# Kernel tuning notes

Measured on AMD Instinct MI355X. Metric: run time of the kernel, lower is better.

Reference implementation:

```python
import jax, jax.numpy as jnp
import numpy as np

B, C, T, F = 16, 64, 400, 64
H = C          # GRU hidden == numUnits == channel
G = 8          # PE groups


def _gru(xs, Wih, Whh, bih, bhh):
    """PyTorch-style GRU, batch_first. xs: [N, T, I]; Wih: [3H, I]; Whh: [3H, H]."""
    gx = jnp.einsum('nti,gi->ntg', xs, Wih) + bih          # [N, T, 3H] input gates precomputed
    Hh = Whh.shape[1]

    def step(h, gxt):
        gh = h @ Whh.T + bhh                               # [N, 3H]
        xr, xz, xn = jnp.split(gxt, 3, axis=-1)
        hr, hz, hn = jnp.split(gh, 3, axis=-1)
        r = jax.nn.sigmoid(xr + hr)
        z = jax.nn.sigmoid(xz + hz)
        n = jnp.tanh(xn + r * hn)
        hn_new = (1.0 - z) * n + z * h
        return hn_new, hn_new

    h0 = jnp.zeros((xs.shape[0], Hh), xs.dtype)
    _, ys = jax.lax.scan(step, h0, jnp.swapaxes(gx, 0, 1))
    return jnp.swapaxes(ys, 0, 1)                          # [N, T, H]


def _ln2(x, g, b, eps=1e-8):
    """LayerNorm over last two dims [width, numUnits]."""
    mu = x.mean(axis=(-2, -1), keepdims=True)
    var = x.var(axis=(-2, -1), keepdims=True)
    return (x - mu) / jnp.sqrt(var + eps) * g + b


def setup_inputs() -> dict:
    key = jax.random.key(0)
    ks = jax.random.split(key, 24)
    s = 0.1

    def rn(k, shape):
        return jax.random.normal(k, shape, dtype=jnp.float32) * s

    return {
        'x': jax.random.normal(ks[0], (B, C, T, F), dtype=jnp.float32),
        # intra bidirectional GRU (input = C = H)
        'intra_Wih_f': rn(ks[1], (3 * H, H)), 'intra_Whh_f': rn(ks[2], (3 * H, H)),
        'intra_bih_f': rn(ks[3], (3 * H,)),   'intra_bhh_f': rn(ks[4], (3 * H,)),
        'intra_Wih_b': rn(ks[5], (3 * H, H)), 'intra_Whh_b': rn(ks[6], (3 * H, H)),
        'intra_bih_b': rn(ks[7], (3 * H,)),   'intra_bhh_b': rn(ks[8], (3 * H,)),
        'intra_fc_W': rn(ks[9], (H, 2 * H)),  'intra_fc_b': rn(ks[10], (H,)),
        'intra_ln_g': jnp.ones((F, H), jnp.float32), 'intra_ln_b': jnp.zeros((F, H), jnp.float32),
        # PE: 8 grouped GRUs + FCs (stacked along group axis)
        'pe_Wih': rn(ks[11], (G, 3 * H, H)), 'pe_Whh': rn(ks[12], (G, 3 * H, H)),
        'pe_bih': rn(ks[13], (G, 3 * H)),    'pe_bhh': rn(ks[14], (G, 3 * H)),
        'pe_fc_W': rn(ks[15], (G, H, H)),    'pe_fc_b': rn(ks[16], (G, H)),
        'pe_ln_g': jnp.ones((F, H), jnp.float32), 'pe_ln_b': jnp.zeros((F, H), jnp.float32),
    }


def _forward(x, intra_Wih_f, intra_Whh_f, intra_bih_f, intra_bhh_f,
             intra_Wih_b, intra_Whh_b, intra_bih_b, intra_bhh_b,
             intra_fc_W, intra_fc_b, intra_ln_g, intra_ln_b,
             pe_Wih, pe_Whh, pe_bih, pe_bhh, pe_fc_W, pe_fc_b, pe_ln_g, pe_ln_b):
    b, c, t, f = x.shape
    xp = jnp.transpose(x, (0, 2, 3, 1))                    # [b, t, f, c]

    # ---- intra path: bidirectional GRU along frequency f ----
    seq = xp.reshape(b * t, f, c)
    fwd = _gru(seq, intra_Wih_f, intra_Whh_f, intra_bih_f, intra_bhh_f)
    bwd = jnp.flip(_gru(jnp.flip(seq, 1), intra_Wih_b, intra_Whh_b, intra_bih_b, intra_bhh_b), 1)
    intra = jnp.concatenate([fwd, bwd], axis=-1) @ intra_fc_W.T + intra_fc_b
    intra = _ln2(intra.reshape(b, t, f, c), intra_ln_g, intra_ln_b)
    intra_out = xp + intra                                  # residual

    # ---- PE: 8 grouped GRUs along time t ----
    y = jnp.transpose(intra_out, (0, 2, 1, 3))             # [b, f, t, c]
    fg = f // G
    yg = y.reshape(b, G, fg, t, c)                         # chunk freq into G groups
    yg = jnp.transpose(yg, (1, 0, 2, 3, 4)).reshape(G, b * fg, t, c)
    rnn = jax.vmap(_gru)(yg, pe_Wih, pe_Whh, pe_bih, pe_bhh)    # [G, b*fg, t, H]
    fc = jnp.einsum('gnth,goh->gnto', rnn, pe_fc_W) + pe_fc_b[:, None, None, :]
    fc = fc.reshape(G, b, fg, t, H).transpose(1, 0, 2, 3, 4).reshape(b, f, t, H)
    inter = _ln2(jnp.transpose(fc, (0, 2, 1, 3)), pe_ln_g, pe_ln_b)   # [b, t, f, c]

    out = intra + inter                                     # note: residual with intra (pre-add), per source
    return jnp.transpose(out, (0, 3, 1, 2))                 # [b, c, t, f]


def reference(x, intra_Wih_f, intra_Whh_f, intra_bih_f, intra_bhh_f,
              intra_Wih_b, intra_Whh_b, intra_bih_b, intra_bhh_b,
              intra_fc_W, intra_fc_b, intra_ln_g, intra_ln_b,
              pe_Wih, pe_Whh, pe_bih, pe_bhh, pe_fc_W, pe_fc_b, pe_ln_g, pe_ln_b):
    return _forward(x, intra_Wih_f, intra_Whh_f, intra_bih_f, intra_bhh_f,
                    intra_Wih_b, intra_Whh_b, intra_bih_b, intra_bhh_b,
                    intra_fc_W, intra_fc_b, intra_ln_g, intra_ln_b,
                    pe_Wih, pe_Whh, pe_bih, pe_bhh, pe_fc_W, pe_fc_b, pe_ln_g, pe_ln_b)
```

## Files before the change

### kernel.cpp

```cpp
#include <hip/hip_runtime.h>
#include <hip/hip_bf16.h>

typedef unsigned short u16;
typedef __attribute__((ext_vector_type(8))) short short8;
typedef __attribute__((ext_vector_type(4))) float f32x4;

#define MFMA16(A,B,C) __builtin_amdgcn_mfma_f32_16x16x32_bf16((A),(B),(C),0,0,0)

#define LDS_FENCE_ACQ()  asm volatile("s_waitcnt lgkmcnt(0)" ::: "memory")
#define LDS_FENCE_REL()  asm volatile("" ::: "memory")

__device__ __forceinline__ float bf2f(u16 u){ return __uint_as_float(((unsigned)u)<<16); }
__device__ __forceinline__ u16 f2bf(float f){
  unsigned x = __float_as_uint(f);
  return (u16)((x + 0x7FFFu + ((x>>16)&1u)) >> 16);
}
__device__ __forceinline__ float sigm(float x){ return __fdividef(1.f, 1.f + __expf(-x)); }
__device__ __forceinline__ float tanh_(float x){ return __fdividef(2.f, 1.f + __expf(-2.f*x)) - 1.f; }
__device__ __forceinline__ short8 ldg8(const u16* p){ return *(const short8*)p; }

struct CvtArgs {
  const void* src[21];
  u16* dst[21];
  int n[21];
};

__global__ __launch_bounds__(256,1) void k_cvt(CvtArgs a)
{
  const u16* d = (const u16*)a.src[0];
  int imp = 0, pl = 0;
#pragma unroll
  for (int i = 0; i < 128; i += 2){
    u16 u = d[i]; int e = (u >> 7) & 0xFF;
    if (u){ if (e >= 104 && e <= 134) pl++; else imp++; }
  }
  bool isf32 = imp > pl;

  int which, i0, stride;
  if (blockIdx.x < 20){ which = blockIdx.x + 1; i0 = threadIdx.x; stride = 256; }
  else { which = 0; i0 = (blockIdx.x - 20)*256 + threadIdx.x; stride = (gridDim.x - 20)*256; }
  int n = a.n[which];
  u16* dst = a.dst[which];
  if (isf32){
    const float* s = (const float*)a.src[which];
    for (int i = i0; i < n; i += stride) dst[i] = f2bf(s[i]);
  } else {
    const u16* s = (const u16*)a.src[which];
    for (int i = i0; i < n; i += stride) dst[i] = s[i];
  }
}

__global__ __launch_bounds__(256,1) void k_transpose(const u16* __restrict__ x, u16* __restrict__ xp)
{
  int nb = blockIdx.x; int b = nb/400, t = nb - b*400;
  int tid = threadIdx.x;
  __shared__ u16 tl[64*66];
  int f0 = (tid & 31) * 2;
#pragma unroll
  for (int p = 0; p < 8; p++){
    int c = p*8 + (tid>>5);
    unsigned u = *(const unsigned*)(x + (((size_t)b*64 + c)*400 + t)*64 + f0);
    *(unsigned*)(tl + c*66 + f0) = u;
  }
  __syncthreads();
  int c0 = (tid & 31) * 2;
  u16* dst = xp + (size_t)nb*4096;
#pragma unroll
  for (int p = 0; p < 8; p++){
    int f = p*8 + (tid>>5);
    unsigned u = (unsigned)tl[c0*66 + f] | ((unsigned)tl[(c0+1)*66 + f] << 16);
    *(unsigned*)(dst + f*64 + c0) = u;
  }
}

__global__ __launch_bounds__(64,1) void k_intra(
    const u16* __restrict__ xp,
    const u16* __restrict__ Wih_f, const u16* __restrict__ Whh_f,
    const u16* __restrict__ bih_f, const u16* __restrict__ bhh_f,
    const u16* __restrict__ Wih_b, const u16* __restrict__ Whh_b,
    const u16* __restrict__ bih_b, const u16* __restrict__ bhh_b,
    u16* __restrict__ yfo, u16* __restrict__ ybo)
{
  int blk = blockIdx.x;
  int dir = blk >= 400;
  int tile = dir ? blk - 400 : blk;
  int n0 = tile * 16;
  const u16* Wih = dir ? Wih_b : Wih_f;
  const u16* Whh = dir ? Whh_b : Whh_f;
  const u16* bih = dir ? bih_b : bih_f;
  const u16* bhh = dir ? bhh_b : bhh_f;
  u16* yo = dir ? ybo : yfo;

  int lane = threadIdx.x;
  int m = lane & 15, q = lane >> 4;

  short8 wrx[4][2], wzx[4][2], wnx[4][2], wrh[4][2], wzh[4][2], wnh[4][2];
#pragma unroll
  for (int nt = 0; nt < 4; nt++){
#pragma unroll
    for (int kc = 0; kc < 2; kc++){
      int co = kc*32 + q*8;
      wrx[nt][kc] = ldg8(Wih + (      nt*16 + m)*64 + co);
      wzx[nt][kc] = ldg8(Wih + ( 64 + nt*16 + m)*64 + co);
      wnx[nt][kc] = ldg8(Wih + (128 + nt*16 + m)*64 + co);
      wrh[nt][kc] = ldg8(Whh + (      nt*16 + m)*64 + co);
      wzh[nt][kc] = ldg8(Whh + ( 64 + nt*16 + m)*64 + co);
      wnh[nt][kc] = ldg8(Whh + (128 + nt*16 + m)*64 + co);
    }
  }
  float br[4], bz[4], bnx_[4], bnh_[4];
#pragma unroll
  for (int nt = 0; nt < 4; nt++){
    int u = nt*16 + m;
    br[nt]   = bf2f(bih[u])     + bf2f(bhh[u]);
    bz[nt]   = bf2f(bih[64+u])  + bf2f(bhh[64+u]);
    bnx_[nt] = bf2f(bih[128+u]);
    bnh_[nt] = bf2f(bhh[128+u]);
  }

  __shared__ u16 hl[16*72];
  float h[4][4];
#pragma unroll
  for (int nt=0;nt<4;nt++){
#pragma unroll
    for (int p=0;p<4;p++) h[nt][p] = 0.f;
  }
  short8 hf0 = {0,0,0,0,0,0,0,0}, hf1 = {0,0,0,0,0,0,0,0};
  int f = dir ? 63 : 0, df = dir ? -1 : 1;
  short8 xf0 = ldg8(xp + ((size_t)(n0+m)*64 + f)*64 + q*8);
  short8 xf1 = ldg8(xp + ((size_t)(n0+m)*64 + f)*64 + 32 + q*8);

  for (int s = 0; s < 64; s++){
    f32x4 ar[4], az[4], anx[4], anh[4];
#pragma unroll
    for (int nt=0;nt<4;nt++){
      ar[nt]  = (f32x4){br[nt],br[nt],br[nt],br[nt]};
      az[nt]  = (f32x4){bz[nt],bz[nt],bz[nt],bz[nt]};
      anx[nt] = (f32x4){bnx_[nt],bnx_[nt],bnx_[nt],bnx_[nt]};
      anh[nt] = (f32x4){bnh_[nt],bnh_[nt],bnh_[nt],bnh_[nt]};
    }
#pragma unroll
    for (int nt=0;nt<4;nt++){
      ar[nt]  = MFMA16(hf0, wrh[nt][0], ar[nt]);
      ar[nt]  = MFMA16(hf1, wrh[nt][1], ar[nt]);
      ar[nt]  = MFMA16(xf0, wrx[nt][0], ar[nt]);
      ar[nt]  = MFMA16(xf1, wrx[nt][1], ar[nt]);
      az[nt]  = MFMA16(hf0, wzh[nt][0], az[nt]);
      az[nt]  = MFMA16(hf1, wzh[nt][1], az[nt]);
      az[nt]  = MFMA16(xf0, wzx[nt][0], az[nt]);
      az[nt]  = MFMA16(xf1, wzx[nt][1], az[nt]);
      anx[nt] = MFMA16(xf0, wnx[nt][0], anx[nt]);
      anx[nt] = MFMA16(xf1, wnx[nt][1], anx[nt]);
      anh[nt] = MFMA16(hf0, wnh[nt][0], anh[nt]);
      anh[nt] = MFMA16(hf1, wnh[nt][1], anh[nt]);
    }
    int fn = f + df;
    if (s < 63){
      xf0 = ldg8(xp + ((size_t)(n0+m)*64 + fn)*64 + q*8);
      xf1 = ldg8(xp + ((size_t)(n0+m)*64 + fn)*64 + 32 + q*8);
    }
#pragma unroll
    for (int nt=0;nt<4;nt++){
#pragma unroll
      for (int p=0;p<4;p++){
        float r  = sigm(ar[nt][p]);
        float z  = sigm(az[nt][p]);
        float n  = tanh_(anx[nt][p] + r*anh[nt][p]);
        float hn = n + z*(h[nt][p] - n);
        h[nt][p] = hn;
        hl[(q*4+p)*72 + nt*16 + m] = f2bf(hn);
      }
    }
    LDS_FENCE_ACQ();
    int sl = lane >> 2, ch = lane & 3;
    short8 y0 = *(const short8*)(hl + sl*72 + ch*16);
    short8 y1 = *(const short8*)(hl + sl*72 + ch*16 + 8);
    *(short8*)(yo + ((size_t)(n0+sl)*64 + f)*64 + ch*16)     = y0;
    *(short8*)(yo + ((size_t)(n0+sl)*64 + f)*64 + ch*16 + 8) = y1;
    hf0 = *(const short8*)(hl + m*72 + q*8);
    hf1 = *(const short8*)(hl + m*72 + 32 + q*8);
    LDS_FENCE_REL();
    f = fn;
  }
}

__global__ __launch_bounds__(256,1) void k_ifc(
  const u16* __restrict__ yf, const u16* __restrict__ yb,
  const u16* __restrict__ fcw, const u16* __restrict__ fcb,
  const u16* __restrict__ lng, const u16* __restrict__ lnb,
  const u16* __restrict__ xp, u16* __restrict__ lnI, u16* __restrict__ iout)
{
  int nb = blockIdx.x; int b = nb/400, t = nb - b*400;
  int tid = threadIdx.x; int wv = tid>>6; int lane = tid&63;
  int m = lane&15, q = lane>>4;
  int rb = nb*64 + wv*16;
  short8 a0 = ldg8(yf + (size_t)(rb+m)*64 + q*8);
  short8 a1 = ldg8(yf + (size_t)(rb+m)*64 + 32 + q*8);
  short8 a2 = ldg8(yb + (size_t)(rb+m)*64 + q*8);
  short8 a3 = ldg8(yb + (size_t)(rb+m)*64 + 32 + q*8);
  f32x4 acc[4];
#pragma unroll
  for (int nt=0;nt<4;nt++){
    float bias = bf2f(fcb[nt*16+m]);
    acc[nt] = (f32x4){bias,bias,bias,bias};
    acc[nt] = MFMA16(a0, ldg8(fcw + (nt*16+m)*128 +      q*8), acc[nt]);
    acc[nt] = MFMA16(a1, ldg8(fcw + (nt*16+m)*128 + 32 + q*8), acc[nt]);
    acc[nt] = MFMA16(a2, ldg8(fcw + (nt*16+m)*128 + 64 + q*8), acc[nt]);
    acc[nt] = MFMA16(a3, ldg8(fcw + (nt*16+m)*128 + 96 + q*8), acc[nt]);
  }
  float s=0.f, s2=0.f;
#pragma unroll
  for (int nt=0;nt<4;nt++){
#pragma unroll
    for (int p=0;p<4;p++){ float v=acc[nt][p]; s+=v; s2+=v*v; }
  }
  for (int o=32;o>0;o>>=1){ s += __shfl_down(s,o); s2 += __shfl_down(s2,o); }
  __shared__ float red[8];
  if (lane==0){ red[wv]=s; red[4+wv]=s2; }
  __syncthreads();
  float S  = red[0]+red[1]+red[2]+red[3];
  float S2 = red[4]+red[5]+red[6]+red[7];
  float mu = S*(1.f/4096.f);
  float rstd = rsqrtf(S2*(1.f/4096.f) - mu*mu + 1e-8f);
#pragma unroll
  for (int nt=0;nt<4;nt++){
#pragma unroll
    for (int p=0;p<4;p++){
      int row = wv*16 + q*4 + p;
      int col = nt*16 + m;
      float v = (acc[nt][p]-mu)*rstd;
      v = v*bf2f(lng[row*64+col]) + bf2f(lnb[row*64+col]);
      lnI[(size_t)nb*4096 + row*64 + col] = f2bf(v);
      float xv = bf2f(xp[(size_t)nb*4096 + row*64 + col]);
      iout[(((size_t)b*64 + row)*400 + t)*64 + col] = f2bf(v + xv);
    }
  }
}

__global__ __launch_bounds__(64,1) void k_gx(const u16* __restrict__ io,
   const u16* __restrict__ pw, const u16* __restrict__ pb, u16* __restrict__ gx)
{
  int r0 = blockIdx.x * 16;
  int seq = r0 / 400;
  int g = (seq & 63) >> 3;
  int lane = threadIdx.x; int m = lane&15, q = lane>>4;
  short8 a0 = ldg8(io + (size_t)(r0+m)*64 + q*8);
  short8 a1 = ldg8(io + (size_t)(r0+m)*64 + 32 + q*8);
  const u16* W = pw + g*12288;
#pragma unroll
  for (int nt=0; nt<12; nt++){
    float bias = bf2f(pb[g*192 + nt*16 + m]);
    f32x4 acc = (f32x4){bias,bias,bias,bias};
    acc = MFMA16(a0, ldg8(W + (nt*16+m)*64 + q*8), acc);
    acc = MFMA16(a1, ldg8(W + (nt*16+m)*64 + 32 + q*8), acc);
#pragma unroll
    for (int p=0;p<4;p++)
      gx[(size_t)(r0 + q*4 + p)*192 + nt*16 + m] = f2bf(acc[p]);
  }
}

__global__ __launch_bounds__(64,1) void k_pe(const u16* __restrict__ gx,
  const u16* __restrict__ whh, const u16* __restrict__ bhh, u16* __restrict__ ype)
{
  int seq = blockIdx.x;
  int g = (seq & 63) >> 3;
  int lane = threadIdx.x;
  int m = lane & 15, q = lane >> 4;

  const u16* W = whh + (size_t)g*12288;
  short8 wr[4][2], wz[4][2], wn[4][2];
#pragma unroll
  for (int nt = 0; nt < 4; nt++){
#pragma unroll
    for (int kc = 0; kc < 2; kc++){
      int co = kc*32 + q*8;
      wr[nt][kc] = ldg8(W + (      nt*16 + m)*64 + co);
      wz[nt][kc] = ldg8(W + ( 64 + nt*16 + m)*64 + co);
      wn[nt][kc] = ldg8(W + (128 + nt*16 + m)*64 + co);
    }
  }
  float br_[4], bz_[4], bn_[4];
#pragma unroll
  for (int nt = 0; nt < 4; nt++){
    br_[nt] = bf2f(bhh[g*192 +       nt*16 + m]);
    bz_[nt] = bf2f(bhh[g*192 + 64  + nt*16 + m]);
    bn_[nt] = bf2f(bhh[g*192 + 128 + nt*16 + m]);
  }

  const u16* gp = gx + (size_t)seq*400*192 + lane;
  u16* yp = ype + (size_t)seq*400*64 + lane;

  u16 cr0 = gp[0],   cz0 = gp[64],  cn0 = gp[128];
  u16 cr1 = gp[192], cz1 = gp[256], cn1 = gp[320];
  gp += 384;

  __shared__ __align__(16) u16 hbuf[128];

  float h = 0.f;
  short8 ah0 = {0,0,0,0,0,0,0,0}, ah1 = {0,0,0,0,0,0,0,0};
  short8 al0 = {0,0,0,0,0,0,0,0}, al1 = {0,0,0,0,0,0,0,0};

  f32x4 accr[4], accz[4], accn[4];
#pragma unroll
  for (int nt=0; nt<4; nt++){
    accr[nt] = (f32x4){br_[nt],br_[nt],br_[nt],br_[nt]};
    accz[nt] = (f32x4){bz_[nt],bz_[nt],bz_[nt],bz_[nt]};
    accn[nt] = (f32x4){bn_[nt],bn_[nt],bn_[nt],bn_[nt]};
  }

#define PE_STEP(CR, CZ, CN, PFOFF, COND)                                      \
  {                                                                           \
    float xr = bf2f(CR), xz = bf2f(CZ), xn = bf2f(CN);                        \
    if (COND){ CR = gp[PFOFF]; CZ = gp[(PFOFF)+64]; CN = gp[(PFOFF)+128]; }   \
    \
    \
    _Pragma("unroll")                                                         \
    for (int nt=0; nt<4; nt++){                                               \
      accr[nt][0] = br_[nt]; accz[nt][0] = bz_[nt]; accn[nt][0] = bn_[nt];    \
    }                                                                         \
    _Pragma("unroll")                                                         \
    for (int nt=0; nt<4; nt++){                                               \
      accr[nt] = MFMA16(ah0, wr[nt][0], accr[nt]);                            \
      accr[nt] = MFMA16(ah1, wr[nt][1], accr[nt]);                            \
      accr[nt] = MFMA16(al0, wr[nt][0], accr[nt]);                            \
      accr[nt] = MFMA16(al1, wr[nt][1], accr[nt]);                            \
      accz[nt] = MFMA16(ah0, wz[nt][0], accz[nt]);                            \
      accz[nt] = MFMA16(ah1, wz[nt][1], accz[nt]);                            \
      accz[nt] = MFMA16(al0, wz[nt][0], accz[nt]);                            \
      accz[nt] = MFMA16(al1, wz[nt][1], accz[nt]);                            \
      accn[nt] = MFMA16(ah0, wn[nt][0], accn[nt]);                            \
      accn[nt] = MFMA16(ah1, wn[nt][1], accn[nt]);                            \
      accn[nt] = MFMA16(al0, wn[nt][0], accn[nt]);                            \
      accn[nt] = MFMA16(al1, wn[nt][1], accn[nt]);                            \
    }                                                                         \
         \
    float ar = accr[0][0]; float az = accz[0][0]; float an = accn[0][0];      \
    ar = (q==1) ? accr[1][0] : ar; az = (q==1) ? accz[1][0] : az;             \
    an = (q==1) ? accn[1][0] : an;                                            \
    ar = (q==2) ? accr[2][0] : ar; az = (q==2) ? accz[2][0] : az;             \
    an = (q==2) ? accn[2][0] : an;                                            \
    ar = (q==3) ? accr[3][0] : ar; az = (q==3) ? accz[3][0] : az;             \
    an = (q==3) ? accn[3][0] : an;                                            \
    float r = sigm(xr + ar);                                                  \
    float z = sigm(xz + az);                                                  \
    float n = tanh_(xn + r*an);                                               \
    h = n + z*(h - n);                                                        \
    u16 hi = f2bf(h);                                                         \
    u16 lo = f2bf(h - bf2f(hi));                                              \
    *yp = hi; yp += 64;                                                       \
    hbuf[lane] = hi;                                                          \
    hbuf[64 + lane] = lo;                                                     \
    LDS_FENCE_ACQ();  \
    ah0 = *(const short8*)(hbuf + q*8);           \
    ah1 = *(const short8*)(hbuf + 32 + q*8);      \
    al0 = *(const short8*)(hbuf + 64 + q*8);                                  \
    al1 = *(const short8*)(hbuf + 96 + q*8);                                  \
    LDS_FENCE_REL();   \
  }

  for (int t = 0; t < 400; t += 2){
    PE_STEP(cr0, cz0, cn0, 0,   t < 398)
    PE_STEP(cr1, cz1, cn1, 192, t < 397)
    gp += 384;
  }
#undef PE_STEP
}

__global__ __launch_bounds__(64,1) void k_pefc(const u16* __restrict__ ype,
  const u16* __restrict__ fw, const u16* __restrict__ fb, u16* __restrict__ fcpe)
{
  int r0 = blockIdx.x * 16;
  int seq = r0 / 400;
  int g = (seq & 63) >> 3;
  int b = seq >> 6, f = seq & 63;
  int tb = r0 - seq*400;
  int lane = threadIdx.x; int m = lane&15, q = lane>>4;
  short8 a0 = ldg8(ype + (size_t)(r0+m)*64 + q*8);
  short8 a1 = ldg8(ype + (size_t)(r0+m)*64 + 32 + q*8);
  const u16* W = fw + g*4096;
#pragma unroll
  for (int nt=0;nt<4;nt++){
    float bias = bf2f(fb[g*64 + nt*16 + m]);
    f32x4 acc = (f32x4){bias,bias,bias,bias};
    acc = MFMA16(a0, ldg8(W + (nt*16+m)*64 + q*8), acc);
    acc = MFMA16(a1, ldg8(W + (nt*16+m)*64 + 32 + q*8), acc);
#pragma unroll
    for (int p=0;p<4;p++){
      int t = tb + q*4 + p;
      fcpe[(((size_t)b*400 + t)*64 + f)*64 + nt*16 + m] = f2bf(acc[p]);
    }
  }
}

__global__ __launch_bounds__(256,1) void k_final(const u16* __restrict__ fcpe,
  const u16* __restrict__ lnI, const u16* __restrict__ g_, const u16* __restrict__ b_,
  float* __restrict__ out)
{
  int nb = blockIdx.x; int b = nb/400, t = nb - b*400;
  int tid = threadIdx.x;
  const u16* src = fcpe + (size_t)nb*4096 + tid*16;
  short8 v0 = ldg8(src), v1 = ldg8(src + 8);
  float v[16];
#pragma unroll
  for (int i=0;i<8;i++){ v[i] = bf2f((u16)v0[i]); v[8+i] = bf2f((u16)v1[i]); }
  float s=0.f, s2=0.f;
#pragma unroll
  for (int i=0;i<16;i++){ s+=v[i]; s2+=v[i]*v[i]; }
  int lane = tid&63, wv = tid>>6;
  for (int o=32;o>0;o>>=1){ s += __shfl_down(s,o); s2 += __shfl_down(s2,o); }
  __shared__ float red[8];
  __shared__ float tr[64*68];
  if (lane==0){ red[wv]=s; red[4+wv]=s2; }
  __syncthreads();
  float S  = red[0]+red[1]+red[2]+red[3];
  float S2 = red[4]+red[5]+red[6]+red[7];
  float mu = S*(1.f/4096.f);
  float rstd = rsqrtf(S2*(1.f/4096.f) - mu*mu + 1e-8f);
  int ff = tid>>2; int c0 = (tid&3)*16;
  const u16* lp = lnI + (size_t)nb*4096 + tid*16;
  short8 l0 = ldg8(lp), l1 = ldg8(lp + 8);
#pragma unroll
  for (int i=0;i<16;i++){
    int c = c0 + i;
    float x = (v[i]-mu)*rstd*bf2f(g_[ff*64+c]) + bf2f(b_[ff*64+c]);
    x += (i<8) ? bf2f((u16)l0[i]) : bf2f((u16)l1[i-8]);
    tr[c*68 + ff] = x;
  }
  __syncthreads();
  int cc = tid>>2, fc = (tid&3)*16;
  float* dst = out + (((size_t)b*64 + cc)*400 + t)*64 + fc;
#pragma unroll
  for (int i=0;i<16;i+=4){
    *(f32x4*)(dst + i) = *(const f32x4*)(tr + cc*68 + fc + i);
  }
}

extern "C" void kernel_launch(void* const* d_in, const int* in_sizes, int n_in,
                              void* d_out, int out_size, void* d_ws, size_t ws_size,
                              hipStream_t stream)
{
  (void)in_sizes; (void)n_in; (void)out_size; (void)ws_size;

  char* ws = (char*)d_ws;
  u16* xp   = (u16*)(ws + 0ull);
  u16* xb   = (u16*)(ws + 52428800ull);
  u16* yf   = (u16*)(ws + 52428800ull);
  u16* yb   = (u16*)(ws + 104857600ull);
  u16* lnI  = (u16*)(ws + 157286400ull);
  u16* iout = (u16*)(ws + 209715200ull);
  u16* gx   = (u16*)(ws + 0ull);
  u16* ype  = (u16*)(ws + 209715200ull);
  u16* fcpe = (u16*)(ws + 0ull);
  u16* wb   = (u16*)(ws + 262144000ull);

  static const int wn[21] = {26214400,
    12288,12288,192,192, 12288,12288,192,192,
    8192,64,4096,4096, 98304,98304,1536,1536, 32768,512,4096,4096};
  int woff[21]; woff[0] = 0;
  int acc = 0;
  for (int i = 1; i <= 20; i++){ woff[i] = acc; acc += wn[i]; }

  CvtArgs ca;
  for (int i = 0; i < 21; i++){
    ca.src[i] = d_in[i];
    ca.n[i] = wn[i];
    ca.dst[i] = (i == 0) ? xb : (wb + woff[i]);
  }

  const u16* iWihf = wb + woff[1];
  const u16* iWhhf = wb + woff[2];
  const u16* ibihf = wb + woff[3];
  const u16* ibhhf = wb + woff[4];
  const u16* iWihb = wb + woff[5];
  const u16* iWhhb = wb + woff[6];
  const u16* ibihb = wb + woff[7];
  const u16* ibhhb = wb + woff[8];
  const u16* fcW   = wb + woff[9];
  const u16* fcB   = wb + woff[10];
  const u16* ilng  = wb + woff[11];
  const u16* ilnb  = wb + woff[12];
  const u16* peWih = wb + woff[13];
  const u16* peWhh = wb + woff[14];
  const u16* pebih = wb + woff[15];
  const u16* pebhh = wb + woff[16];
  const u16* pefcW = wb + woff[17];
  const u16* pefcb = wb + woff[18];
  const u16* pelng = wb + woff[19];
  const u16* pelnb = wb + woff[20];

  k_cvt<<<dim3(2068), dim3(256), 0, stream>>>(ca);
  k_transpose<<<dim3(6400), dim3(256), 0, stream>>>(xb, xp);
  k_intra<<<dim3(800), dim3(64), 0, stream>>>(xp, iWihf, iWhhf, ibihf, ibhhf,
                                              iWihb, iWhhb, ibihb, ibhhb, yf, yb);
  k_ifc<<<dim3(6400), dim3(256), 0, stream>>>(yf, yb, fcW, fcB, ilng, ilnb, xp, lnI, iout);
  k_gx<<<dim3(25600), dim3(64), 0, stream>>>(iout, peWih, pebih, gx);
  k_pe<<<dim3(1024), dim3(64), 0, stream>>>(gx, peWhh, pebhh, ype);
  k_pefc<<<dim3(25600), dim3(64), 0, stream>>>(ype, pefcW, pefcb, fcpe);
  k_final<<<dim3(6400), dim3(256), 0, stream>>>(fcpe, lnI, pelng, pelnb, (float*)d_out);
}
```

Measured before the change: 1.283 ms.

## Batch four PE GRU sequences per wavefront using MFMA rows

```diff
diff --git a/kernel.cpp b/kernel.cpp
--- a/kernel.cpp
+++ b/kernel.cpp
@@ -262,8 +262,9 @@
 __global__ __launch_bounds__(64,1) void k_pe(const u16* __restrict__ gx,
   const u16* __restrict__ whh, const u16* __restrict__ bhh, u16* __restrict__ ype)
 {
-  int seq = blockIdx.x;
-  int g = (seq & 63) >> 3;
+  int blk = blockIdx.x;
+  int s0 = blk << 2;
+  int g = (s0 & 63) >> 3;
   int lane = threadIdx.x;
   int m = lane & 15, q = lane >> 4;
 
@@ -287,39 +288,50 @@
     bn_[nt] = bf2f(bhh[g*192 + 128 + nt*16 + m]);
   }
 
-  const u16* gp = gx + (size_t)seq*400*192 + lane;
-  u16* yp = ype + (size_t)seq*400*64 + lane;
-
-  u16 cr0 = gp[0],   cz0 = gp[64],  cn0 = gp[128];
-  u16 cr1 = gp[192], cz1 = gp[256], cn1 = gp[320];
-  gp += 384;
-
-  __shared__ __align__(16) u16 hbuf[128];
-
-  float h = 0.f;
+  const u16* gp[4];
+  u16* yp[4];
+#pragma unroll
+  for (int p = 0; p < 4; p++){
+    gp[p] = gx + (size_t)(s0+p)*76800 + lane;
+    yp[p] = ype + (size_t)(s0+p)*25600 + lane;
+  }
+  u16 crA[4], czA[4], cnA[4], crB[4], czB[4], cnB[4];
+#pragma unroll
+  for (int p = 0; p < 4; p++){
+    crA[p] = gp[p][0];   czA[p] = gp[p][64];  cnA[p] = gp[p][128];
+    crB[p] = gp[p][192]; czB[p] = gp[p][256]; cnB[p] = gp[p][320];
+    gp[p] += 384;
+  }
+
+  __shared__ __align__(16) u16 hbuf[4][2][64];
+
+  float hprev[4] = {0.f, 0.f, 0.f, 0.f};
   short8 ah0 = {0,0,0,0,0,0,0,0}, ah1 = {0,0,0,0,0,0,0,0};
   short8 al0 = {0,0,0,0,0,0,0,0}, al1 = {0,0,0,0,0,0,0,0};
 
-  f32x4 accr[4], accz[4], accn[4];
-#pragma unroll
-  for (int nt=0; nt<4; nt++){
-    accr[nt] = (f32x4){br_[nt],br_[nt],br_[nt],br_[nt]};
-    accz[nt] = (f32x4){bz_[nt],bz_[nt],bz_[nt],bz_[nt]};
-    accn[nt] = (f32x4){bn_[nt],bn_[nt],bn_[nt],bn_[nt]};
-  }
-
 #define PE_STEP(CR, CZ, CN, PFOFF, COND)                                      \
   {                                                                           \
-    float xr = bf2f(CR), xz = bf2f(CZ), xn = bf2f(CN);                        \
-    if (COND){ CR = gp[PFOFF]; CZ = gp[(PFOFF)+64]; CN = gp[(PFOFF)+128]; }   \
-    \
-    \
+    float xr[4], xz[4], xn[4];                                                \
     _Pragma("unroll")                                                         \
-    for (int nt=0; nt<4; nt++){                                               \
-      accr[nt][0] = br_[nt]; accz[nt][0] = bz_[nt]; accn[nt][0] = bn_[nt];    \
+    for (int p = 0; p < 4; p++){                                              \
+      xr[p] = bf2f(CR[p]); xz[p] = bf2f(CZ[p]); xn[p] = bf2f(CN[p]);          \
+    }                                                                         \
+    if (COND){                                                                \
+      _Pragma("unroll")                                                       \
+      for (int p = 0; p < 4; p++){                                            \
+        CR[p] = gp[p][PFOFF]; CZ[p] = gp[p][(PFOFF)+64];                      \
+        CN[p] = gp[p][(PFOFF)+128];                                           \
+      }                                                                       \
+    }                                                                         \
+    f32x4 accr[4], accz[4], accn[4];                                          \
+    _Pragma("unroll")                                                         \
+    for (int nt = 0; nt < 4; nt++){                                           \
+      accr[nt] = (f32x4){br_[nt],br_[nt],br_[nt],br_[nt]};                    \
+      accz[nt] = (f32x4){bz_[nt],bz_[nt],bz_[nt],bz_[nt]};                    \
+      accn[nt] = (f32x4){bn_[nt],bn_[nt],bn_[nt],bn_[nt]};                    \
     }                                                                         \
     _Pragma("unroll")                                                         \
-    for (int nt=0; nt<4; nt++){                                               \
+    for (int nt = 0; nt < 4; nt++){                                           \
       accr[nt] = MFMA16(ah0, wr[nt][0], accr[nt]);                            \
       accr[nt] = MFMA16(ah1, wr[nt][1], accr[nt]);                            \
       accr[nt] = MFMA16(al0, wr[nt][0], accr[nt]);                            \
@@ -333,35 +345,39 @@
       accn[nt] = MFMA16(al0, wn[nt][0], accn[nt]);                            \
       accn[nt] = MFMA16(al1, wn[nt][1], accn[nt]);                            \
     }                                                                         \
-         \
-    float ar = accr[0][0]; float az = accz[0][0]; float an = accn[0][0];      \
-    ar = (q==1) ? accr[1][0] : ar; az = (q==1) ? accz[1][0] : az;             \
-    an = (q==1) ? accn[1][0] : an;                                            \
-    ar = (q==2) ? accr[2][0] : ar; az = (q==2) ? accz[2][0] : az;             \
-    an = (q==2) ? accn[2][0] : an;                                            \
-    ar = (q==3) ? accr[3][0] : ar; az = (q==3) ? accz[3][0] : az;             \
-    an = (q==3) ? accn[3][0] : an;                                            \
-    float r = sigm(xr + ar);                                                  \
-    float z = sigm(xz + az);                                                  \
-    float n = tanh_(xn + r*an);                                               \
-    h = n + z*(h - n);                                                        \
-    u16 hi = f2bf(h);                                                         \
-    u16 lo = f2bf(h - bf2f(hi));                                              \
-    *yp = hi; yp += 64;                                                       \
-    hbuf[lane] = hi;                                                          \
-    hbuf[64 + lane] = lo;                                                     \
-    LDS_FENCE_ACQ();  \
-    ah0 = *(const short8*)(hbuf + q*8);           \
-    ah1 = *(const short8*)(hbuf + 32 + q*8);      \
-    al0 = *(const short8*)(hbuf + 64 + q*8);                                  \
-    al1 = *(const short8*)(hbuf + 96 + q*8);                                  \
-    LDS_FENCE_REL();   \
+            \
+    _Pragma("unroll")                                                         \
+    for (int p = 0; p < 4; p++){                                              \
+      float ar = accr[0][p], az = accz[0][p], an = accn[0][p];                \
+      ar = (q==1) ? accr[1][p] : ar; az = (q==1) ? accz[1][p] : az;           \
+      an = (q==1) ? accn[1][p] : an;                                          \
+      ar = (q==2) ? accr[2][p] : ar; az = (q==2) ? accz[2][p] : az;           \
+      an = (q==2) ? accn[2][p] : an;                                          \
+      ar = (q==3) ? accr[3][p] : ar; az = (q==3) ? accz[3][p] : az;           \
+      an = (q==3) ? accn[3][p] : an;                                          \
+      float r = sigm(xr[p] + ar);                                             \
+      float z = sigm(xz[p] + az);                                             \
+      float n = tanh_(xn[p] + r*an);                                          \
+      float hn = n + z*(hprev[p] - n);                                        \
+      hprev[p] = hn;                                                          \
+      u16 hi = f2bf(hn);                                                      \
+      *(yp[p]) = hi; yp[p] += 64;                                             \
+      hbuf[p][0][lane] = hi;                                                  \
+      hbuf[p][1][lane] = f2bf(hn - bf2f(hi));                                 \
+    }                                                                         \
+    LDS_FENCE_ACQ();          \
+    ah0 = *(const short8*)&hbuf[m & 3][0][q*8];                               \
+    ah1 = *(const short8*)&hbuf[m & 3][0][32 + q*8];                          \
+    al0 = *(const short8*)&hbuf[m & 3][1][q*8];                               \
+    al1 = *(const short8*)&hbuf[m & 3][1][32 + q*8];                          \
+    LDS_FENCE_REL();           \
   }
 
   for (int t = 0; t < 400; t += 2){
-    PE_STEP(cr0, cz0, cn0, 0,   t < 398)
-    PE_STEP(cr1, cz1, cn1, 192, t < 397)
-    gp += 384;
+    PE_STEP(crA, czA, cnA, 0,   t < 398)
+    PE_STEP(crB, czB, cnB, 192, t < 397)
+#pragma unroll
+    for (int p = 0; p < 4; p++) gp[p] += 384;
   }
 #undef PE_STEP
 }
@@ -494,7 +510,7 @@
                                               iWihb, iWhhb, ibihb, ibhhb, yf, yb);
   k_ifc<<<dim3(6400), dim3(256), 0, stream>>>(yf, yb, fcW, fcB, ilng, ilnb, xp, lnI, iout);
   k_gx<<<dim3(25600), dim3(64), 0, stream>>>(iout, peWih, pebih, gx);
-  k_pe<<<dim3(1024), dim3(64), 0, stream>>>(gx, peWhh, pebhh, ype);
+  k_pe<<<dim3(256), dim3(64), 0, stream>>>(gx, peWhh, pebhh, ype);
   k_pefc<<<dim3(25600), dim3(64), 0, stream>>>(ype, pefcW, pefcb, fcpe);
   k_final<<<dim3(6400), dim3(256), 0, stream>>>(fcpe, lnI, pelng, pelnb, (float*)d_out);
 }
```

After: 1.309 ms. About the same (+2.0%).
